# Kernel optimization log

Hardware: AMD Instinct MI355X
Metric: run time of the kernel (lower is better)

## Reference

```python
import jax, jax.numpy as jnp
import numpy as np

# Dimensions (match input_specs / init_kwargs)
B, T, M, H, E, K = 4, 2048, 1024, 2048, 8, 2
CAP_FACTOR = 1.0  # tutel default capacity_factor
S = B * T
C = int(K * CAP_FACTOR * ((S + E - 1) // E))  # per-expert capacity (tutel Top-k gate)


def setup_inputs() -> dict:
    key = jax.random.key(0)
    ks = jax.random.split(key, 4)
    x = jax.random.normal(ks[0], (B, T, M), jnp.float32)
    wg = jax.random.normal(ks[1], (M, E), jnp.float32) / np.sqrt(M)
    w1 = jax.random.normal(ks[2], (E, M, H), jnp.float32) / np.sqrt(M)
    b1 = jnp.zeros((E, H), jnp.float32)
    w2 = jax.random.normal(ks[3], (E, H, M), jnp.float32) / np.sqrt(H)
    b2 = jnp.zeros((E, M), jnp.float32)
    return {"x": x, "wg": wg, "w1": w1, "b1": b1, "w2": w2, "b2": b2}


def reference(x, wg, w1, b1, w2, b2):
    xf = x.reshape(S, M)
    # ---- Top-k gate (fp32 gate) ----
    logits = xf.astype(jnp.float32) @ wg                 # [S, E]
    scores = jax.nn.softmax(logits, axis=-1)
    topv, topi = jax.lax.top_k(scores, K)                # [S, K]
    gates = topv / (jnp.sum(topv, axis=-1, keepdims=True) + 1e-9)  # normalized top-k gates

    # ---- Dispatch into [E, C, M] buffer with capacity-based token dropping ----
    buf = jnp.zeros((E, C, M), xf.dtype)
    offset = jnp.zeros((E,), jnp.int32)  # tokens already placed per expert (previous slots)
    pos_list, keep_list = [], []
    for j in range(K):  # small fixed loop over top-k slots
        e = topi[:, j]                                   # [S]
        m = jax.nn.one_hot(e, E, dtype=jnp.int32)        # [S, E]
        pos = jnp.sum(jnp.cumsum(m, axis=0) * m, axis=1) - 1 + offset[e]  # position within expert
        offset = offset + jnp.sum(m, axis=0)
        keep = pos < C                                   # drop tokens over capacity
        posc = jnp.minimum(pos, C - 1)
        buf = buf.at[e, posc].add(xf * keep[:, None].astype(xf.dtype))
        pos_list.append(posc)
        keep_list.append(keep)

    # ---- Grouped expert FFN: relu(x W1 + b1) W2 + b2 ----
    h = jax.nn.relu(jnp.einsum('ecm,emh->ech', buf, w1) + b1[:, None, :])  # [E, C, H]
    y = jnp.einsum('ech,ehm->ecm', h, w2) + b2[:, None, :]                 # [E, C, M]

    # ---- Combine with gate weights ----
    out = jnp.zeros_like(xf)
    for j in range(K):
        g = gates[:, j] * keep_list[j].astype(xf.dtype)
        out = out + g[:, None] * y[topi[:, j], pos_list[j]]

    out = out.reshape(B, T, M)
    # result = log_softmax(sum over model_dim, over token dim)
    return jax.nn.log_softmax(jnp.sum(out, axis=2), axis=1)   # [B, T]
```

## Files before the change

### kernel.cpp

```cpp
#include <hip/hip_runtime.h>
#include <hip/hip_bf16.h>
#include <cstdint>
#include <cstddef>

constexpr int Bb = 4;
constexpr int Tt = 2048;
constexpr int Mm = 1024;
constexpr int Hh = 2048;
constexpr int Ee = 8;
constexpr int Ss = Bb * Tt;
constexpr int Cc = 2048;

typedef __attribute__((ext_vector_type(4))) float f32x4;
typedef __attribute__((ext_vector_type(8))) short bf16x8;

__device__ inline void load_lds16(const void* g, void* l) {
    __builtin_amdgcn_global_load_lds(
        (const __attribute__((address_space(1))) unsigned int*)g,
        (__attribute__((address_space(3))) unsigned int*)l, 16, 0, 0);
}

__global__ __launch_bounds__(256) void k_prep(
    const float* __restrict__ w1, const float* __restrict__ w2, const float* __restrict__ b2,
    const float* __restrict__ x, const float* __restrict__ wg,
    __hip_bfloat16* __restrict__ w1t, float* __restrict__ w2sum, float* __restrict__ b2sum,
    int* __restrict__ esel, float* __restrict__ gates, __hip_bfloat16* __restrict__ xbf) {
    int bid = blockIdx.x;
    int t = threadIdx.x;
    if (bid < 4096) {
        __shared__ float tile[64][65];
        int e = bid >> 9, m0 = ((bid >> 5) & 15) * 64, h0 = (bid & 31) * 64;
        const float* src = w1 + (size_t)e * Mm * Hh;
        #pragma unroll
        for (int i = 0; i < 4; i++) {
            int idx = t + i * 256;
            int r = idx >> 4, c4 = idx & 15;
            float4 v = *(const float4*)(src + (size_t)(m0 + r) * Hh + h0 + c4 * 4);
            tile[r][c4 * 4 + 0] = v.x; tile[r][c4 * 4 + 1] = v.y;
            tile[r][c4 * 4 + 2] = v.z; tile[r][c4 * 4 + 3] = v.w;
        }
        __syncthreads();
        __hip_bfloat16* dst = w1t + (size_t)e * Hh * Mm;
        #pragma unroll
        for (int i = 0; i < 2; i++) {
            int idx = t + i * 256;
            int r = idx >> 3, c8 = idx & 7;
            __hip_bfloat16 tmp[8];
            #pragma unroll
            for (int k = 0; k < 8; k++) tmp[k] = __float2bfloat16(tile[c8 * 8 + k][r]);
            uint4 vv; __builtin_memcpy(&vv, tmp, 16);
            *(uint4*)(dst + (size_t)(h0 + r) * Mm + m0 + c8 * 8) = vv;
        }
    } else if (bid < 8192) {
        int wave = t >> 6, lane = t & 63;
        int r = (bid - 4096) * 4 + wave;
        const float4* p = (const float4*)(w2 + (size_t)r * Mm);
        float s = 0.f;
        #pragma unroll
        for (int i = 0; i < 4; i++) { float4 v = p[lane + i * 64]; s += v.x + v.y + v.z + v.w; }
        #pragma unroll
        for (int off = 32; off; off >>= 1) s += __shfl_down(s, off);
        if (lane == 0) w2sum[r] = s;
    } else if (bid == 8192) {
        int wave = t >> 6, lane = t & 63;
        int e = wave * 2 + (lane >> 5);
        int l = lane & 31;
        const float4* p = (const float4*)(b2 + (size_t)e * Mm);
        float s = 0.f;
        #pragma unroll
        for (int i = 0; i < 8; i++) { float4 v = p[l + i * 32]; s += v.x + v.y + v.z + v.w; }
        #pragma unroll
        for (int off = 16; off; off >>= 1) s += __shfl_down(s, off);
        if (l == 0) b2sum[e] = s;
    } else {
        int gb = bid - 8193;
        int s = (gb * 256 + t) >> 6;
        int lane = t & 63;
        const float4* xr = (const float4*)(x + (size_t)s * Mm);
        const float4* wgr = (const float4*)wg;
        float acc[8];
        #pragma unroll
        for (int e = 0; e < 8; e++) acc[e] = 0.f;
        #pragma unroll
        for (int i = 0; i < 4; i++) {
            float4 xv = xr[lane + i * 64];
            __hip_bfloat16 tb[4];
            tb[0] = __float2bfloat16(xv.x); tb[1] = __float2bfloat16(xv.y);
            tb[2] = __float2bfloat16(xv.z); tb[3] = __float2bfloat16(xv.w);
            uint2 u; __builtin_memcpy(&u, tb, 8);
            *(uint2*)(xbf + (size_t)s * Mm + (lane + i * 64) * 4) = u;
            int mbase = (lane + i * 64) * 4;
            #pragma unroll
            for (int k = 0; k < 4; k++) {
                int m = mbase + k;
                float xm = (k == 0) ? xv.x : (k == 1) ? xv.y : (k == 2) ? xv.z : xv.w;
                float4 w0 = wgr[m * 2], w1v = wgr[m * 2 + 1];
                acc[0] += xm * w0.x;  acc[1] += xm * w0.y;  acc[2] += xm * w0.z;  acc[3] += xm * w0.w;
                acc[4] += xm * w1v.x; acc[5] += xm * w1v.y; acc[6] += xm * w1v.z; acc[7] += xm * w1v.w;
            }
        }
        #pragma unroll
        for (int off = 32; off; off >>= 1)
            #pragma unroll
            for (int e = 0; e < 8; e++) acc[e] += __shfl_down(acc[e], off);
        if (lane == 0) {
            float mx = acc[0];
            #pragma unroll
            for (int e = 1; e < 8; e++) mx = fmaxf(mx, acc[e]);
            float p[8], se = 0.f;
            #pragma unroll
            for (int e = 0; e < 8; e++) { p[e] = expf(acc[e] - mx); se += p[e]; }
            float inv = 1.f / se;
            #pragma unroll
            for (int e = 0; e < 8; e++) p[e] *= inv;
            int i0 = 0; float v0 = p[0];
            #pragma unroll
            for (int e = 1; e < 8; e++) if (p[e] > v0) { v0 = p[e]; i0 = e; }
            int i1 = -1; float v1 = -1.f;
            #pragma unroll
            for (int e = 0; e < 8; e++) if (e != i0 && p[e] > v1) { v1 = p[e]; i1 = e; }
            float den = v0 + v1 + 1e-9f;
            esel[s] = i0; esel[Ss + s] = i1;
            gates[s] = v0 / den; gates[Ss + s] = v1 / den;
        }
    }
}

__global__ __launch_bounds__(256) void k_posA(const int* __restrict__ esel,
                                              int* __restrict__ lrank, int* __restrict__ blockhist) {
    int b = blockIdx.x, t = threadIdx.x;
    int d = b * 256 + t;
    int e = esel[d];
    int wave = t >> 6, lane = t & 63;
    __shared__ int wh[4][8];
    unsigned long long mymask = 0;
    #pragma unroll
    for (int q = 0; q < 8; q++) {
        unsigned long long m = __ballot(e == q);
        if (q == e) mymask = m;
        if (lane == 0) wh[wave][q] = (int)__popcll(m);
    }
    __syncthreads();
    int prefix = (int)__popcll(mymask & ((1ull << lane) - 1ull));
    for (int w = 0; w < wave; w++) prefix += wh[w][e];
    lrank[d] = prefix;
    if (t < 8) blockhist[b * 8 + t] = wh[0][t] + wh[1][t] + wh[2][t] + wh[3][t];
}

__global__ __launch_bounds__(512) void k_posB(const int* __restrict__ blockhist,
                                              int* __restrict__ blockbase) {
    int t = threadIdx.x;
    int wave = t >> 6, lane = t & 63;
    int v = blockhist[lane * 8 + wave];
    int x = v;
    #pragma unroll
    for (int off = 1; off < 64; off <<= 1) {
        int y = __shfl_up(x, off);
        if (lane >= off) x += y;
    }
    blockbase[lane * 8 + wave] = x - v;
}

__global__ __launch_bounds__(256) void k_sidx(const int* __restrict__ esel,
                                              const int* __restrict__ lrank,
                                              const int* __restrict__ blockbase,
                                              int* __restrict__ pos, int* __restrict__ srcidx) {
    int d = blockIdx.x * 256 + threadIdx.x;
    int e = esel[d];
    int p = blockbase[(d >> 8) * 8 + e] + lrank[d];
    pos[d] = p;
    if (p < Cc) srcidx[e * Cc + p] = d & (Ss - 1);
}

__global__ __launch_bounds__(512, 2) void k_gemm(
    const __hip_bfloat16* __restrict__ xbf, const int* __restrict__ srcidx,
    const __hip_bfloat16* __restrict__ w1t,
    const float* __restrict__ b1, const float* __restrict__ w2sum,
    float* __restrict__ rowsum) {
    __shared__ __align__(16) __hip_bfloat16 As[4][256 * 32];
    __shared__ __align__(16) __hip_bfloat16 Bs[4][256 * 32];
    int bid = blockIdx.x;
    int e = bid & 7;
    int tile = bid >> 3;
    int cb = tile >> 3, hb = tile & 7;
    int c0 = cb * 256, h0 = hb * 256;
    int t = threadIdx.x;
    int wave = t >> 6, lane = t & 63;
    int wm = wave >> 2;
    int wn = wave & 3;
    int r16 = lane & 15, quad = lane >> 4;
    int r_s = t >> 2;
    int qd = ((t & 3) - ((t >> 3) & 3)) & 3;
    int s0 = srcidx[e * Cc + c0 + r_s];
    int s1 = srcidx[e * Cc + c0 + 128 + r_s];
    const __hip_bfloat16* a0 = xbf + (size_t)s0 * Mm + qd * 8;
    const __hip_bfloat16* a1 = xbf + (size_t)s1 * Mm + qd * 8;
    const __hip_bfloat16* Bp = w1t + (size_t)e * Hh * Mm;
    const __hip_bfloat16* b0 = Bp + (size_t)(h0 + r_s) * Mm + qd * 8;
    const __hip_bfloat16* b1p = Bp + (size_t)(h0 + 128 + r_s) * Mm + qd * 8;
    int fo = r16 * 4 + ((quad + (r16 >> 1)) & 3);
    f32x4 acc[8][4];
    #pragma unroll
    for (int i = 0; i < 8; i++)
        #pragma unroll
        for (int j = 0; j < 4; j++) acc[i][j] = (f32x4){0.f, 0.f, 0.f, 0.f};

    #pragma unroll
    for (int p = 0; p < 3; p++) {
        int k0 = p * 32;
        load_lds16(a0 + k0,  As[p] + t * 8);
        load_lds16(a1 + k0,  As[p] + (512 + t) * 8);
        load_lds16(b0 + k0,  Bs[p] + t * 8);
        load_lds16(b1p + k0, Bs[p] + (512 + t) * 8);
    }

    for (int j = 0; j < 29; ++j) {
        __builtin_amdgcn_sched_barrier(0);
        asm volatile("s_waitcnt vmcnt(8)" ::: "memory");
        __builtin_amdgcn_s_barrier();
        __builtin_amdgcn_sched_barrier(0);
        {
            int b = (j + 3) & 3;
            int k0 = (j + 3) * 32;
            load_lds16(a0 + k0,  As[b] + t * 8);
            load_lds16(a1 + k0,  As[b] + (512 + t) * 8);
            load_lds16(b0 + k0,  Bs[b] + t * 8);
            load_lds16(b1p + k0, Bs[b] + (512 + t) * 8);
        }
        const __hip_bfloat16* Ar = As[j & 3];
        const __hip_bfloat16* Br = Bs[j & 3];
        bf16x8 bfr[4];
        #pragma unroll
        for (int ni = 0; ni < 4; ni++)
            bfr[ni] = *(const bf16x8*)(Br + ((wn * 4 + ni) * 64 + fo) * 8);
        __builtin_amdgcn_s_setprio(1);
        #pragma unroll
        for (int mi = 0; mi < 8; mi++) {
            bf16x8 af = *(const bf16x8*)(Ar + ((wm * 8 + mi) * 64 + fo) * 8);
            #pragma unroll
            for (int ni = 0; ni < 4; ni++)
                acc[mi][ni] = __builtin_amdgcn_mfma_f32_16x16x32_bf16(af, bfr[ni], acc[mi][ni], 0, 0, 0);
        }
        __builtin_amdgcn_s_setprio(0);
    }
    #pragma unroll
    for (int j = 29; j < 32; ++j) {
        __builtin_amdgcn_sched_barrier(0);
        if (j == 29)      asm volatile("s_waitcnt vmcnt(8)" ::: "memory");
        else if (j == 30) asm volatile("s_waitcnt vmcnt(4)" ::: "memory");
        else              asm volatile("s_waitcnt vmcnt(0)" ::: "memory");
        __builtin_amdgcn_s_barrier();
        __builtin_amdgcn_sched_barrier(0);
        const __hip_bfloat16* Ar = As[j & 3];
        const __hip_bfloat16* Br = Bs[j & 3];
        bf16x8 bfr[4];
        #pragma unroll
        for (int ni = 0; ni < 4; ni++)
            bfr[ni] = *(const bf16x8*)(Br + ((wn * 4 + ni) * 64 + fo) * 8);
        __builtin_amdgcn_s_setprio(1);
        #pragma unroll
        for (int mi = 0; mi < 8; mi++) {
            bf16x8 af = *(const bf16x8*)(Ar + ((wm * 8 + mi) * 64 + fo) * 8);
            #pragma unroll
            for (int ni = 0; ni < 4; ni++)
                acc[mi][ni] = __builtin_amdgcn_mfma_f32_16x16x32_bf16(af, bfr[ni], acc[mi][ni], 0, 0, 0);
        }
        __builtin_amdgcn_s_setprio(0);
    }
    __builtin_amdgcn_sched_barrier(0);

    float b1v[4], wsv[4];
    #pragma unroll
    for (int ni = 0; ni < 4; ni++) {
        int hg = h0 + wn * 64 + ni * 16 + r16;
        b1v[ni] = b1[e * Hh + hg];
        wsv[ni] = w2sum[e * Hh + hg];
    }
    #pragma unroll
    for (int mi = 0; mi < 8; mi++) {
        #pragma unroll
        for (int r = 0; r < 4; r++) {
            float val = 0.f;
            #pragma unroll
            for (int ni = 0; ni < 4; ni++) {
                float sv = acc[mi][ni][r] + b1v[ni];
                val += fmaxf(sv, 0.f) * wsv[ni];
            }
            #pragma unroll
            for (int off = 1; off < 16; off <<= 1) val += __shfl_xor(val, off);
            if (r16 == 0) {
                int cg = c0 + wm * 128 + mi * 16 + quad * 4 + r;
                atomicAdd(&rowsum[e * Cc + cg], val);
            }
        }
    }
}

__global__ __launch_bounds__(256) void k_combine(
    const int* __restrict__ esel, const int* __restrict__ pos,
    const float* __restrict__ gates, const float* __restrict__ rowsum,
    const float* __restrict__ b2sum, float* __restrict__ vals) {
    int s = blockIdx.x * 256 + threadIdx.x;
    float acc = 0.f;
    #pragma unroll
    for (int j = 0; j < 2; j++) {
        int d = j * Ss + s;
        int p = pos[d];
        if (p < Cc) {
            int ee = esel[d];
            acc += gates[d] * (rowsum[ee * Cc + p] + b2sum[ee]);
        }
    }
    vals[s] = acc;
}

__global__ __launch_bounds__(1024) void k_lsm(const float* __restrict__ vals,
                                              float* __restrict__ out) {
    int b = blockIdx.x; int t = threadIdx.x;
    __shared__ float red[1024];
    float v0 = vals[b * Tt + t];
    float v1 = vals[b * Tt + t + 1024];
    float m = fmaxf(v0, v1);
    red[t] = m; __syncthreads();
    for (int st = 512; st; st >>= 1) { if (t < st) red[t] = fmaxf(red[t], red[t + st]); __syncthreads(); }
    float mx = red[0];
    __syncthreads();
    float se = expf(v0 - mx) + expf(v1 - mx);
    red[t] = se; __syncthreads();
    for (int st = 512; st; st >>= 1) { if (t < st) red[t] += red[t + st]; __syncthreads(); }
    float lse = logf(red[0]);
    out[b * Tt + t] = v0 - mx - lse;
    out[b * Tt + t + 1024] = v1 - mx - lse;
}

extern "C" void kernel_launch(void* const* d_in, const int* in_sizes, int n_in,
                              void* d_out, int out_size, void* d_ws, size_t ws_size,
                              hipStream_t stream) {
    const float* x  = (const float*)d_in[0];
    const float* wg = (const float*)d_in[1];
    const float* w1 = (const float*)d_in[2];
    const float* b1 = (const float*)d_in[3];
    const float* w2 = (const float*)d_in[4];
    const float* b2 = (const float*)d_in[5];
    float* out = (float*)d_out;

    char* ws = (char*)d_ws;
    size_t off = 0;
    auto alloc = [&](size_t bytes) -> void* {
        void* p = ws + off;
        off += (bytes + 255) & ~(size_t)255;
        return p;
    };
    float* rowsum   = (float*)alloc((size_t)Ee * Cc * 4 + (size_t)Ee * Cc * 4);
    int*   srcidx   = (int*)(rowsum + (size_t)Ee * Cc);
    float* w2sum    = (float*)alloc((size_t)Ee * Hh * 4);
    float* b2sum    = (float*)alloc(Ee * 4);
    int*   esel     = (int*)alloc((size_t)2 * Ss * 4);
    int*   lrank    = (int*)alloc((size_t)2 * Ss * 4);
    int*   blockhist= (int*)alloc((size_t)64 * 8 * 4);
    int*   blockbase= (int*)alloc((size_t)64 * 8 * 4);
    int*   pos      = (int*)alloc((size_t)2 * Ss * 4);
    float* gates    = (float*)alloc((size_t)2 * Ss * 4);
    __hip_bfloat16* xbf = (__hip_bfloat16*)alloc((size_t)Ss * Mm * 2);
    __hip_bfloat16* w1t = (__hip_bfloat16*)alloc((size_t)Ee * Hh * Mm * 2);

    hipMemsetAsync(rowsum, 0, (size_t)2 * Ee * Cc * 4, stream);
    k_prep<<<10241, 256, 0, stream>>>(w1, w2, b2, x, wg, w1t, w2sum, b2sum, esel, gates, xbf);
    k_posA<<<64, 256, 0, stream>>>(esel, lrank, blockhist);
    k_posB<<<1, 512, 0, stream>>>(blockhist, blockbase);
    k_sidx<<<64, 256, 0, stream>>>(esel, lrank, blockbase, pos, srcidx);
    k_gemm<<<512, 512, 0, stream>>>(xbf, srcidx, w1t, b1, w2sum, rowsum);
    float* vals = (float*)lrank;
    k_combine<<<32, 256, 0, stream>>>(esel, pos, gates, rowsum, b2sum, vals);
    k_lsm<<<Bb, 1024, 0, stream>>>(vals, out);
}
```

Baseline: 307.1 us.

## Restructure GEMM main loop into 8-phase ping-pong schedule with split half-tile MFMA phases

Replaces the 4-buffer K-loop (one barrier per 32-wide k-step) with a double-buffered 64-wide K schedule split into phases. Each phase covers half of the M fragments, issues a fraction of the next global->LDS loads, and separates the LDS reads from the MFMA cluster with barriers. This is meant to interleave memory issue with matrix math more finely and to balance the waves. In exchange it adds two barriers per phase, roughly four times as many as before, and keeps only about two k-steps of prefetch depth.

```diff
diff --git a/kernel.cpp b/kernel.cpp
--- a/kernel.cpp
+++ b/kernel.cpp
@@ -177,8 +177,8 @@
     const __hip_bfloat16* __restrict__ w1t,
     const float* __restrict__ b1, const float* __restrict__ w2sum,
     float* __restrict__ rowsum) {
-    __shared__ __align__(16) __hip_bfloat16 As[4][256 * 32];
-    __shared__ __align__(16) __hip_bfloat16 Bs[4][256 * 32];
+    __shared__ __align__(16) __hip_bfloat16 A_lds[2][2][8192];
+    __shared__ __align__(16) __hip_bfloat16 B_lds[2][2][8192];
     int bid = blockIdx.x;
     int e = bid & 7;
     int tile = bid >> 3;
@@ -199,75 +199,76 @@
     const __hip_bfloat16* b0 = Bp + (size_t)(h0 + r_s) * Mm + qd * 8;
     const __hip_bfloat16* b1p = Bp + (size_t)(h0 + 128 + r_s) * Mm + qd * 8;
     int fo = r16 * 4 + ((quad + (r16 >> 1)) & 3);
+    int lsl = t * 8, hsl = (512 + t) * 8;
     f32x4 acc[8][4];
     #pragma unroll
     for (int i = 0; i < 8; i++)
         #pragma unroll
         for (int j = 0; j < 4; j++) acc[i][j] = (f32x4){0.f, 0.f, 0.f, 0.f};
 
-    #pragma unroll
-    for (int p = 0; p < 3; p++) {
-        int k0 = p * 32;
-        load_lds16(a0 + k0,  As[p] + t * 8);
-        load_lds16(a1 + k0,  As[p] + (512 + t) * 8);
-        load_lds16(b0 + k0,  Bs[p] + t * 8);
-        load_lds16(b1p + k0, Bs[p] + (512 + t) * 8);
-    }
-
-    for (int j = 0; j < 29; ++j) {
-        __builtin_amdgcn_sched_barrier(0);
-        asm volatile("s_waitcnt vmcnt(8)" ::: "memory");
-        __builtin_amdgcn_s_barrier();
-        __builtin_amdgcn_sched_barrier(0);
-        {
-            int b = (j + 3) & 3;
-            int k0 = (j + 3) * 32;
-            load_lds16(a0 + k0,  As[b] + t * 8);
-            load_lds16(a1 + k0,  As[b] + (512 + t) * 8);
-            load_lds16(b0 + k0,  Bs[b] + t * 8);
-            load_lds16(b1p + k0, Bs[b] + (512 + t) * 8);
-        }
-        const __hip_bfloat16* Ar = As[j & 3];
-        const __hip_bfloat16* Br = Bs[j & 3];
-        bf16x8 bfr[4];
-        #pragma unroll
-        for (int ni = 0; ni < 4; ni++)
-            bfr[ni] = *(const bf16x8*)(Br + ((wn * 4 + ni) * 64 + fo) * 8);
-        __builtin_amdgcn_s_setprio(1);
-        #pragma unroll
-        for (int mi = 0; mi < 8; mi++) {
-            bf16x8 af = *(const bf16x8*)(Ar + ((wm * 8 + mi) * 64 + fo) * 8);
-            #pragma unroll
-            for (int ni = 0; ni < 4; ni++)
-                acc[mi][ni] = __builtin_amdgcn_mfma_f32_16x16x32_bf16(af, bfr[ni], acc[mi][ni], 0, 0, 0);
-        }
-        __builtin_amdgcn_s_setprio(0);
-    }
-    #pragma unroll
-    for (int j = 29; j < 32; ++j) {
-        __builtin_amdgcn_sched_barrier(0);
-        if (j == 29)      asm volatile("s_waitcnt vmcnt(8)" ::: "memory");
-        else if (j == 30) asm volatile("s_waitcnt vmcnt(4)" ::: "memory");
-        else              asm volatile("s_waitcnt vmcnt(0)" ::: "memory");
-        __builtin_amdgcn_s_barrier();
-        __builtin_amdgcn_sched_barrier(0);
-        const __hip_bfloat16* Ar = As[j & 3];
-        const __hip_bfloat16* Br = Bs[j & 3];
-        bf16x8 bfr[4];
-        #pragma unroll
-        for (int ni = 0; ni < 4; ni++)
-            bfr[ni] = *(const bf16x8*)(Br + ((wn * 4 + ni) * 64 + fo) * 8);
-        __builtin_amdgcn_s_setprio(1);
-        #pragma unroll
-        for (int mi = 0; mi < 8; mi++) {
-            bf16x8 af = *(const bf16x8*)(Ar + ((wm * 8 + mi) * 64 + fo) * 8);
-            #pragma unroll
-            for (int ni = 0; ni < 4; ni++)
-                acc[mi][ni] = __builtin_amdgcn_mfma_f32_16x16x32_bf16(af, bfr[ni], acc[mi][ni], 0, 0, 0);
-        }
-        __builtin_amdgcn_s_setprio(0);
-    }
-    __builtin_amdgcn_sched_barrier(0);
+#define STAGE_A(DB, KK, T) do { \
+    load_lds16(a0 + (T) * 64 + (KK) * 32, &A_lds[DB][KK][lsl]); \
+    load_lds16(a1 + (T) * 64 + (KK) * 32, &A_lds[DB][KK][hsl]); } while (0);
+#define STAGE_B(DB, KK, T) do { \
+    load_lds16(b0 + (T) * 64 + (KK) * 32, &B_lds[DB][KK][lsl]); \
+    load_lds16(b1p + (T) * 64 + (KK) * 32, &B_lds[DB][KK][hsl]); } while (0);
+#define NOSTAGE
+#define VM8 asm volatile("s_waitcnt vmcnt(8)" ::: "memory");
+#define VM4 asm volatile("s_waitcnt vmcnt(4)" ::: "memory");
+#define VM0 asm volatile("s_waitcnt vmcnt(0)" ::: "memory");
+#define VMNONE
+
+#define PHASE(DB, KK, MH, STAGE_STMT, VM_STMT) do { \
+    __builtin_amdgcn_sched_barrier(0); \
+    bf16x8 paf[4], pbf[4]; \
+    const __hip_bfloat16* Ab_ = &A_lds[DB][KK][0]; \
+    const __hip_bfloat16* Bb_ = &B_lds[DB][KK][0]; \
+    _Pragma("unroll") \
+    for (int q_ = 0; q_ < 4; q_++) { \
+        paf[q_] = *(const bf16x8*)(Ab_ + ((wm * 8 + (MH) * 4 + q_) * 64 + fo) * 8); \
+        pbf[q_] = *(const bf16x8*)(Bb_ + ((wn * 4 + q_) * 64 + fo) * 8); \
+    } \
+    STAGE_STMT \
+    __builtin_amdgcn_s_barrier(); \
+    asm volatile("s_waitcnt lgkmcnt(0)" ::: "memory"); \
+    __builtin_amdgcn_sched_barrier(0); \
+    __builtin_amdgcn_s_setprio(1); \
+    _Pragma("unroll") \
+    for (int mi_ = 0; mi_ < 4; mi_++) \
+        _Pragma("unroll") \
+        for (int ni_ = 0; ni_ < 4; ni_++) \
+            acc[(MH) * 4 + mi_][ni_] = __builtin_amdgcn_mfma_f32_16x16x32_bf16( \
+                paf[mi_], pbf[ni_], acc[(MH) * 4 + mi_][ni_], 0, 0, 0); \
+    __builtin_amdgcn_s_setprio(0); \
+    __builtin_amdgcn_sched_barrier(0); \
+    VM_STMT \
+    __builtin_amdgcn_s_barrier(); \
+} while (0)
+
+    STAGE_A(0, 0, 0) STAGE_B(0, 0, 0) STAGE_A(0, 1, 0) STAGE_B(0, 1, 0)
+    STAGE_A(1, 0, 1) STAGE_B(1, 0, 1)
+    asm volatile("s_waitcnt vmcnt(8)" ::: "memory");
+    __builtin_amdgcn_s_barrier();
+
+    for (int i = 0; i < 7; ++i) {
+        int T1 = 2 * i + 1, T2 = 2 * i + 2, T3 = 2 * i + 3;
+        PHASE(0, 0, 0, STAGE_A(1, 1, T1), VMNONE);
+        PHASE(0, 0, 1, STAGE_B(1, 1, T1), VM8);
+        PHASE(0, 1, 0, STAGE_A(0, 0, T2), VMNONE);
+        PHASE(0, 1, 1, STAGE_B(0, 0, T2), VM8);
+        PHASE(1, 0, 0, STAGE_A(0, 1, T2), VMNONE);
+        PHASE(1, 0, 1, STAGE_B(0, 1, T2), VM8);
+        PHASE(1, 1, 0, STAGE_A(1, 0, T3), VMNONE);
+        PHASE(1, 1, 1, STAGE_B(1, 0, T3), VM8);
+    }
+    PHASE(0, 0, 0, STAGE_A(1, 1, 15), VMNONE);
+    PHASE(0, 0, 1, STAGE_B(1, 1, 15), VM8);
+    PHASE(0, 1, 0, NOSTAGE, VMNONE);
+    PHASE(0, 1, 1, NOSTAGE, VM4);
+    PHASE(1, 0, 0, NOSTAGE, VMNONE);
+    PHASE(1, 0, 1, NOSTAGE, VM0);
+    PHASE(1, 1, 0, NOSTAGE, VMNONE);
+    PHASE(1, 1, 1, NOSTAGE, VMNONE);
 
     float b1v[4], wsv[4];
     #pragma unroll
```

Result: faster. 287.9 us (-6.3%).
